# Kernel optimization log

Hardware: AMD Instinct MI355X
Metric: run time of the kernel (lower is better)

Reference implementation:

```python
import jax, jax.numpy as jnp
import numpy as np

SR = 22050
FRAME_LENGTH = 64
ATTENUATE_GAIN = 0.02


def upsample_linear(x, scale):
    """torch nn.Upsample(mode='linear', align_corners=False) along last axis."""
    T = x.shape[-1]
    S = T * scale
    # source coordinate for each output sample (half-pixel convention), clamped
    coords = jnp.clip((jnp.arange(S, dtype=jnp.float32) + 0.5) / scale - 0.5, 0.0, T - 1)
    i0 = jnp.floor(coords).astype(jnp.int32)
    i1 = jnp.minimum(i0 + 1, T - 1)
    w = (coords - i0).astype(x.dtype)
    return x[..., i0] * (1.0 - w) + x[..., i1] * w


def setup_inputs() -> dict:
    key = jax.random.key(0)
    k1, k2, k3 = jax.random.split(key, 3)
    B, T, P, STR = 16, 1000, 64, 6
    # fundamental frequencies in [50, 450] Hz so high partials hit the Nyquist mask
    six_f0 = jax.random.uniform(k1, (B, T, STR), dtype=jnp.float32) * 400.0 + 50.0
    c = jax.random.uniform(k2, (STR, B, P, T), dtype=jnp.float32)
    a = jax.random.uniform(k3, (STR, B, T), dtype=jnp.float32)
    return {"six_f0": six_f0, "c": c, "a": a, "string_idx": 1}


def reference(six_f0, c, a, string_idx):
    sidx = string_idx - 1
    fundamentals = six_f0[..., sidx]        # (B, T)
    c_bank = c[sidx]                        # (B, P, T)
    loudness = a[sidx]                      # (B, T)
    P = c_bank.shape[1]

    partial_mult = jnp.arange(1, P + 1, dtype=jnp.float32)[:, None]   # (P, 1)
    f0_bank = fundamentals[:, None, :] * partial_mult                  # (B, P, T)
    mask = (f0_bank < SR / 2).astype(c_bank.dtype)
    c_masked = c_bank * mask

    f0_up = upsample_linear(f0_bank, FRAME_LENGTH)                     # (B, P, S)
    phase = jnp.cumsum(f0_up / SR, axis=2)
    a_up = upsample_linear(c_masked, FRAME_LENGTH)                     # (B, P, S)
    sinusoid_bank = jnp.sin(2.0 * np.pi * phase) * a_up * ATTENUATE_GAIN

    loudness_up = upsample_linear(loudness, FRAME_LENGTH)              # (B, S)
    return jnp.sum(sinusoid_bank, axis=1) * loudness_up                # (B, S)
```

## Files before the change

kernel.cpp:

```cpp
#include <hip/hip_runtime.h>
#include <math.h>

constexpr int B = 16, T = 1000, P = 64, STR = 6, SCALE = 64;
constexpr int S = T * SCALE;
constexpr int SEGS_PER_BLK = 16;
constexpr int NF = 17;
constexpr int NBLK = 63;
#define NYQ 11025.0f
#define INV_SR (1.0f / 22050.0f)
#define INV_SR_D (1.0 / 22050.0)

__device__ __forceinline__ float fracf_(float x) {
#if __has_builtin(__builtin_amdgcn_fractf)
  return __builtin_amdgcn_fractf(x);
#else
  return x - floorf(x);
#endif
}
__device__ __forceinline__ float sin2pi(float r) {
#if __has_builtin(__builtin_amdgcn_sinf)
  return __builtin_amdgcn_sinf(r);
#else
  return __sinf(r * 6.28318530717958647692f);
#endif
}
__device__ __forceinline__ float cos2pi(float r) {
#if __has_builtin(__builtin_amdgcn_cosf)
  return __builtin_amdgcn_cosf(r);
#else
  return __cosf(r * 6.28318530717958647692f);
#endif
}

__global__ __launch_bounds__(256) void k_fused(
    const float* __restrict__ six_f0, const float* __restrict__ c,
    const float* __restrict__ a, const int* __restrict__ sidx_p,
    float* __restrict__ out) {
  const int b = blockIdx.y;
  const int G0 = blockIdx.x * SEGS_PER_BLK;
  const int fbase = G0 - 1;
  const int tid = threadIdx.x;
  const int sidx = sidx_p[0] - 1;
  const float* f0row = six_f0 + (size_t)b * T * STR + sidx;
  const float* cb = c + (size_t)sidx * B * P * T;
  const float* loud = a + (size_t)sidx * B * T + (size_t)b * T;

  __shared__ float Fsh[NF];
  __shared__ float Lsh[NF];
  __shared__ double wtot[4];
  __shared__ float ampsT[P][NF + 1];

  if (tid < NF) {
    int f = min(max(fbase + tid, 0), T - 1);
    Fsh[tid] = f0row[(size_t)f * STR];
  } else if (tid < 2 * NF) {
    int i = tid - NF;
    int f = min(max(fbase + i, 0), T - 1);
    Lsh[i] = loud[f];
  }
  double psum = 0.0;
  for (int t = 1 + tid; t <= G0 - 2; t += 256)
    psum += (double)f0row[(size_t)t * STR];
  __syncthreads();

  for (int i = tid; i < P * NF; i += 256) {
    int p = i / NF, fl = i - p * NF;
    int f = min(max(fbase + fl, 0), T - 1);
    float F = Fsh[fl];
    float cv = cb[((size_t)b * P + p) * T + f];
    ampsT[p][fl] = ((float)(p + 1) * F < NYQ) ? cv : 0.0f;
  }
  {
    double v = psum;
    for (int off = 32; off >= 1; off >>= 1) v += __shfl_down(v, off, 64);
    if ((tid & 63) == 0) wtot[tid >> 6] = v;
  }
  __syncthreads();

  const double Ssum = wtot[0] + wtot[1] + wtot[2] + wtot[3];
  const double F0d = (double)f0row[0];
  double baseHz;
  if (G0 == 0)
    baseHz = 0.0;
  else if (G0 == 1)
    baseHz = 32.0 * F0d;
  else
    baseHz = 32.0 * F0d + 32.0 * (F0d + 2.0 * Ssum + (double)Fsh[0]);

  const int m = tid >> 4;
  const int seg = G0 + m;
  for (int g = G0; g < seg; ++g) {
    double ss;
    if (g == 0)
      ss = 32.0 * F0d;
    else if (g >= T)
      ss = 32.0 * (double)Fsh[g - 1 - fbase];
    else
      ss = 32.0 * ((double)Fsh[g - 1 - fbase] + (double)Fsh[g - fbase]);
    baseHz += ss;
  }
  double phd = baseHz * INV_SR_D;
  phd -= floor(phd);
  const float base = (float)phd;

  const int q = tid & 15;
  const int lo_l = m;
  const float Flo = Fsh[lo_l];
  const float Fhi = Fsh[lo_l + 1];
  const float Llo = Lsh[lo_l];
  const float dL = Lsh[lo_l + 1] - Llo;
  const float dF = Fhi - Flo;
  const int kadj = (seg == 0) ? -32 : 0;
  const int kp = q * 4;

  float wj[4], twoC[4], scur[4], sprev[4], accj[4];
#pragma unroll
  for (int j = 0; j < 4; ++j) {
    int k = kp + j + kadj;
    float kf1 = (float)(k + 1);
    float local = (kf1 * Flo + dF * kf1 * kf1 * (1.0f / 128.0f)) * INV_SR;
    float phi = fracf_(base + local);
    wj[j] = ((float)k + 0.5f) * (1.0f / 64.0f);
    twoC[j] = 2.0f * cos2pi(phi);
    scur[j] = sin2pi(phi);
    sprev[j] = 0.0f;
    accj[j] = 0.0f;
  }

  const float Fmn = fminf(Flo, Fhi);
  const int pmax = min(P, (int)(NYQ / Fmn) + 1);

  const float* row = &ampsT[0][lo_l];
#pragma unroll 2
  for (int p = 0; p < pmax; ++p) {
    float a0 = row[p * (NF + 1)];
    float a1 = row[p * (NF + 1) + 1];
    float d = a1 - a0;
#pragma unroll
    for (int j = 0; j < 4; ++j) {
      float amp = fmaf(wj[j], d, a0);
      accj[j] = fmaf(amp, scur[j], accj[j]);
      float sn = fmaf(twoC[j], scur[j], -sprev[j]);
      sprev[j] = scur[j];
      scur[j] = sn;
    }
  }

  bool live = (seg < 1000) ? !(seg == 0 && q < 8) : (seg == 1000 && q < 8);
  if (live) {
    int s0 = seg * 64 - 32 + kp;
    float4 r;
    r.x = accj[0] * 0.02f * fmaf(wj[0], dL, Llo);
    r.y = accj[1] * 0.02f * fmaf(wj[1], dL, Llo);
    r.z = accj[2] * 0.02f * fmaf(wj[2], dL, Llo);
    r.w = accj[3] * 0.02f * fmaf(wj[3], dL, Llo);
    *(float4*)(out + (size_t)b * S + s0) = r;
  }
}

extern "C" void kernel_launch(void* const* d_in, const int* in_sizes, int n_in,
                              void* d_out, int out_size, void* d_ws,
                              size_t ws_size, hipStream_t stream) {
  const float* six_f0 = (const float*)d_in[0];
  const float* c = (const float*)d_in[1];
  const float* a = (const float*)d_in[2];
  const int* sidx = (const int*)d_in[3];
  float* out = (float*)d_out;

  hipLaunchKernelGGL(k_fused, dim3(NBLK, B), dim3(256), 0, stream, six_f0, c,
                     a, sidx, out);
}
```

Baseline: 86.38 us.

## Precompute per-segment phase offsets with a separate prefix-scan kernel

Adds a small kernel that computes a double-precision prefix sum of the fundamental frequency per batch and writes the wrapped phase offset for every segment to workspace. The main kernel then loads its base phase directly instead of having every block redundantly sum all preceding frames and run a serial per-thread loop. This removes repeated strided global reads, a reduction and a barrier from the main kernel, at the cost of an extra kernel launch and a dependency through global memory.

```diff
diff --git a/kernel.cpp b/kernel.cpp
--- a/kernel.cpp
+++ b/kernel.cpp
@@ -6,6 +6,7 @@
 constexpr int SEGS_PER_BLK = 16;
 constexpr int NF = 17;
 constexpr int NBLK = 63;
+constexpr int WS_PITCH = 1024;
 #define NYQ 11025.0f
 #define INV_SR (1.0f / 22050.0f)
 #define INV_SR_D (1.0 / 22050.0)
@@ -32,10 +33,65 @@
 #endif
 }
 
+__global__ __launch_bounds__(256) void k_scan(
+    const float* __restrict__ six_f0, const int* __restrict__ sidx_p,
+    float* __restrict__ basef) {
+  const int b = blockIdx.x;
+  const int tid = threadIdx.x;
+  const int sidx = sidx_p[0] - 1;
+  const float* f0row = six_f0 + (size_t)b * T * STR + sidx;
+
+  __shared__ double PSsh[T];
+  __shared__ double wtot[4];
+
+  const int t0 = tid * 4;
+  double v0, v1, v2, v3, s;
+  {
+    float f0 = (t0 + 0 < T) ? f0row[(size_t)(t0 + 0) * STR] : 0.0f;
+    float f1 = (t0 + 1 < T) ? f0row[(size_t)(t0 + 1) * STR] : 0.0f;
+    float f2 = (t0 + 2 < T) ? f0row[(size_t)(t0 + 2) * STR] : 0.0f;
+    float f3 = (t0 + 3 < T) ? f0row[(size_t)(t0 + 3) * STR] : 0.0f;
+    v0 = (double)f0;
+    v1 = v0 + (double)f1;
+    v2 = v1 + (double)f2;
+    v3 = v2 + (double)f3;
+    s = v3;
+  }
+  double wscan = s;
+#pragma unroll
+  for (int off = 1; off < 64; off <<= 1) {
+    double n = __shfl_up(wscan, off, 64);
+    if ((tid & 63) >= off) wscan += n;
+  }
+  if ((tid & 63) == 63) wtot[tid >> 6] = wscan;
+  __syncthreads();
+  double wbase = 0.0;
+  {
+    const int w = tid >> 6;
+    if (w > 0) wbase += wtot[0];
+    if (w > 1) wbase += wtot[1];
+    if (w > 2) wbase += wtot[2];
+  }
+  const double excl = wbase + (wscan - s);
+  if (t0 + 0 < T) PSsh[t0 + 0] = excl + v0;
+  if (t0 + 1 < T) PSsh[t0 + 1] = excl + v1;
+  if (t0 + 2 < T) PSsh[t0 + 2] = excl + v2;
+  if (t0 + 3 < T) PSsh[t0 + 3] = excl + v3;
+  __syncthreads();
+
+  for (int g = tid; g <= T; g += 256) {
+    double ps1 = (g >= 1) ? PSsh[g - 1] : 0.0;
+    double ps2 = (g >= 2) ? PSsh[g - 2] : 0.0;
+    double phd = 32.0 * (ps1 + ps2) * INV_SR_D;
+    phd -= floor(phd);
+    basef[(size_t)b * WS_PITCH + g] = (float)phd;
+  }
+}
+
 __global__ __launch_bounds__(256) void k_fused(
     const float* __restrict__ six_f0, const float* __restrict__ c,
     const float* __restrict__ a, const int* __restrict__ sidx_p,
-    float* __restrict__ out) {
+    const float* __restrict__ basef, float* __restrict__ out) {
   const int b = blockIdx.y;
   const int G0 = blockIdx.x * SEGS_PER_BLK;
   const int fbase = G0 - 1;
@@ -47,8 +103,11 @@
 
   __shared__ float Fsh[NF];
   __shared__ float Lsh[NF];
-  __shared__ double wtot[4];
   __shared__ float ampsT[P][NF + 1];
+
+  const int m = tid >> 4;
+  const int seg = G0 + m;
+  const float base = basef[(size_t)b * WS_PITCH + min(seg, T)];
 
   if (tid < NF) {
     int f = min(max(fbase + tid, 0), T - 1);
@@ -58,9 +117,6 @@
     int f = min(max(fbase + i, 0), T - 1);
     Lsh[i] = loud[f];
   }
-  double psum = 0.0;
-  for (int t = 1 + tid; t <= G0 - 2; t += 256)
-    psum += (double)f0row[(size_t)t * STR];
   __syncthreads();
 
   for (int i = tid; i < P * NF; i += 256) {
@@ -70,38 +126,7 @@
     float cv = cb[((size_t)b * P + p) * T + f];
     ampsT[p][fl] = ((float)(p + 1) * F < NYQ) ? cv : 0.0f;
   }
-  {
-    double v = psum;
-    for (int off = 32; off >= 1; off >>= 1) v += __shfl_down(v, off, 64);
-    if ((tid & 63) == 0) wtot[tid >> 6] = v;
-  }
-  __syncthreads();
-
-  const double Ssum = wtot[0] + wtot[1] + wtot[2] + wtot[3];
-  const double F0d = (double)f0row[0];
-  double baseHz;
-  if (G0 == 0)
-    baseHz = 0.0;
-  else if (G0 == 1)
-    baseHz = 32.0 * F0d;
-  else
-    baseHz = 32.0 * F0d + 32.0 * (F0d + 2.0 * Ssum + (double)Fsh[0]);
-
-  const int m = tid >> 4;
-  const int seg = G0 + m;
-  for (int g = G0; g < seg; ++g) {
-    double ss;
-    if (g == 0)
-      ss = 32.0 * F0d;
-    else if (g >= T)
-      ss = 32.0 * (double)Fsh[g - 1 - fbase];
-    else
-      ss = 32.0 * ((double)Fsh[g - 1 - fbase] + (double)Fsh[g - fbase]);
-    baseHz += ss;
-  }
-  double phd = baseHz * INV_SR_D;
-  phd -= floor(phd);
-  const float base = (float)phd;
+  __syncthreads();
 
   const int q = tid & 15;
   const int lo_l = m;
@@ -166,7 +191,10 @@
   const float* a = (const float*)d_in[2];
   const int* sidx = (const int*)d_in[3];
   float* out = (float*)d_out;
-
+  float* basef = (float*)d_ws;
+
+  hipLaunchKernelGGL(k_scan, dim3(B), dim3(256), 0, stream, six_f0, sidx,
+                     basef);
   hipLaunchKernelGGL(k_fused, dim3(NBLK, B), dim3(256), 0, stream, six_f0, c,
-                     a, sidx, out);
-}
+                     a, sidx, basef, out);
+}
```

Result: no change. 87.18 us (+0.9%).
